# Kernel tuning notes

Measured on AMD Instinct MI355X. Metric: run time of the kernel, lower is better.

The kernel has to match this reference:

```python
import jax, jax.numpy as jnp
import numpy as np

N_NODES = 25000
N_EDGES = 400000
FEAT = 128
N_CH = 32
FEAT_OUT = 128
N_OUT = 32
P = 6
NUM_NEIGHBORS = 16.0
INV_SQRT3 = 1.0 / np.sqrt(3.0)


def _envelope_coeffs(n0, n1):
    # unique poly of degree n0+n1+1 with f(0)=1, derivs 1..n0 zero at 0,
    # f(1)=0 and derivs 1..n1 zero at 1  (== e3nn.poly_envelope(n0, n1))
    D = n0 + n1 + 1
    powers = np.arange(n0 + 1, D + 1)
    m = n1 + 1
    A = np.zeros((m, m)); b = np.zeros(m)
    for k in range(m):
        for ji, j in enumerate(powers):
            A[k, ji] = np.prod(np.arange(j, j - k, -1.0))  # falling factorial j!/(j-k)!
        b[k] = -1.0 if k == 0 else 0.0
    return powers, np.linalg.solve(A, b)

_POW, _COEF = _envelope_coeffs(P - 1, 2)


def envelope(d):
    poly = 1.0 + sum(float(c) * d ** int(j) for j, c in zip(_POW, _COEF))
    return jnp.where(d < 1.0, poly, 0.0)


def safe_norm(x, axis=None):
    x2 = jnp.sum(x ** 2, axis=axis)
    return jnp.where(x2 == 0, 1, x2) ** 0.5


def setup_inputs():
    key = jax.random.key(0)
    ks = jax.random.split(key, 10)
    x = jax.random.normal(ks[0], (N_EDGES, FEAT), jnp.float32)
    V = jax.random.normal(ks[1], (N_EDGES, N_CH, 4), jnp.float32)
    r = 0.3 * jax.random.normal(ks[2], (N_EDGES, 3), jnp.float32)  # norms mostly < cutoff 1
    Y = jax.random.normal(ks[3], (N_EDGES, 4), jnp.float32)        # irreps 0e+1o
    edge_src = jax.random.randint(ks[4], (N_EDGES,), 0, N_NODES)
    W1 = jax.random.normal(ks[5], (FEAT, N_CH), jnp.float32)
    W2a = jax.random.normal(ks[6], (FEAT + 2 * N_CH, FEAT_OUT), jnp.float32)
    W2b = jax.random.normal(ks[7], (FEAT_OUT, FEAT_OUT), jnp.float32)
    W2c = jax.random.normal(ks[8], (FEAT_OUT, FEAT_OUT), jnp.float32)
    Wlin = jax.random.normal(ks[9], (2 * N_CH, N_OUT), jnp.float32)
    return dict(x=x, V=V, r=r, Y=Y, edge_src=edge_src,
                W1=W1, W2a=W2a, W2b=W2b, W2c=W2c, Wlin=Wlin)


def reference(x, V, r, Y, edge_src, W1, W2a, W2b, W2c, Wlin):
    E, F = x.shape
    n = V.shape[1]
    d = safe_norm(r, axis=1)                               # (E,)
    # edge MLP (e3nn MLP with one layer, no activation; 1/sqrt(fan_in) weight norm)
    w = (x @ W1) / jnp.sqrt(F)                             # (E, n)
    wY = w[:, :, None] * Y[:, None, :]                     # (E, n, 4) irreps 0e+1o
    # index_add over edge_src with map_back=True
    agg = jax.ops.segment_sum(wY, edge_src, num_segments=N_NODES)
    wY = agg[edge_src] / jnp.sqrt(NUM_NEIGHBORS)           # (E, n, 4)
    # CG tensor product wY (x) V, filter_ir_out = 0e + 1o  (component normalization)
    a_s, a_v = wY[..., 0], wY[..., 1:4]
    b_s, b_v = V[..., 0], V[..., 1:4]
    s1 = a_s * b_s                                         # 0e x 0e -> 0e
    s2 = jnp.sum(a_v * b_v, axis=-1) * INV_SQRT3           # 1o x 1o -> 0e
    v1 = a_s[..., None] * b_v                              # 0e x 1o -> 1o
    v2 = a_v * b_s[..., None]                              # 1o x 0e -> 1o
    # scalars: filter(keep='0e').axis_to_mul() -> (E, 2n), concat with x
    scalars = jnp.stack([s1, s2], axis=-1).reshape(E, 2 * n)
    h = jnp.concatenate([x, scalars], axis=1)              # (E, F + 2n)
    # 3-layer silu MLP, no output activation, 1/sqrt(fan_in) weight norm
    h = jax.nn.silu((h @ W2a) / jnp.sqrt(F + 2 * n))
    h = jax.nn.silu((h @ W2b) / jnp.sqrt(FEAT_OUT))
    h = (h @ W2c) / jnp.sqrt(FEAT_OUT)
    x_out = envelope(d)[:, None] * h                       # (E, FEAT_OUT)
    # V: axis_to_mul -> (E, 2n x 1o); equivariant Linear -> n_out x 1o; mul_to_axis
    Vv = jnp.stack([v1, v2], axis=2).reshape(E, 2 * n, 3)
    V_out = jnp.einsum('eui,uv->evi', Vv, Wlin) / jnp.sqrt(2 * n)  # (E, n_out, 3)
    return x_out, V_out
```

## Files before the change

### kernel.cpp

```cpp
#include <hip/hip_runtime.h>

#define NE 400000
#define NNODES 25000

typedef __attribute__((ext_vector_type(8))) short short8;
typedef __attribute__((ext_vector_type(4))) float f32x4;

#define W2A_H 0
#define W2A_L 24576
#define W2B_H 49152
#define W2B_L 65536
#define W2C_H 81920
#define W2C_L 98304
#define WLIN_H 114688
#define WLIN_L 116736
#define W1_H   118784
#define W1_L   122880

__device__ __forceinline__ unsigned short f2bf(float f) {
  unsigned int u = __float_as_uint(f);
  unsigned int r = u + 0x7fffu + ((u >> 16) & 1u);
  return (unsigned short)(r >> 16);
}
__device__ __forceinline__ float bf2f(unsigned short h) {
  return __uint_as_float(((unsigned int)h) << 16);
}
__device__ __forceinline__ unsigned int cvtpk(float lo, float hi) {
  unsigned int r;
  asm("v_cvt_pk_bf16_f32 %0, %1, %2" : "=v"(r) : "v"(lo), "v"(hi));
  return r;
}
__device__ __forceinline__ float fsilu(float z) {
  return z * __builtin_amdgcn_rcpf(1.f + __expf(-z));
}

__global__ __launch_bounds__(256) void kscanA(const int* __restrict__ cnt,
                                              int* __restrict__ start,
                                              int* __restrict__ sums) {
  __shared__ int wtot[4];
  const int t = threadIdx.x, lane = t & 63, wid = t >> 6;
  const int idx = blockIdx.x * 256 + t;
  int v = (idx < NNODES) ? cnt[idx] : 0;
  int incl = v;
  #pragma unroll
  for (int off = 1; off < 64; off <<= 1) {
    int u = __shfl_up(incl, off, 64);
    if (lane >= off) incl += u;
  }
  if (lane == 63) wtot[wid] = incl;
  __syncthreads();
  int woff = 0;
  #pragma unroll
  for (int i = 0; i < 4; ++i)
    if (i < wid) woff += wtot[i];
  int excl = incl - v + woff;
  if (idx < NNODES) start[idx] = excl;
  if (t == 255) sums[blockIdx.x] = excl + v;
}

__global__ __launch_bounds__(64) void kscanB(int* __restrict__ sums) {
  const int lane = threadIdx.x & 63;
  int a = (lane < 98) ? sums[lane] : 0;
  int b = (64 + lane < 98) ? sums[64 + lane] : 0;
  int ia = a;
  #pragma unroll
  for (int off = 1; off < 64; off <<= 1) {
    int u = __shfl_up(ia, off, 64);
    if (lane >= off) ia += u;
  }
  int total_a = __shfl(ia, 63, 64);
  int ib = b;
  #pragma unroll
  for (int off = 1; off < 64; off <<= 1) {
    int u = __shfl_up(ib, off, 64);
    if (lane >= off) ib += u;
  }
  if (lane < 98) sums[lane] = ia - a;
  if (64 + lane < 98) sums[64 + lane] = total_a + ib - b;
}

__global__ __launch_bounds__(256) void kscanC(const int* __restrict__ sums,
                                              int* __restrict__ start,
                                              int* __restrict__ cursor) {
  const int idx = blockIdx.x * 256 + threadIdx.x;
  if (idx < NNODES) {
    int s = start[idx] + sums[blockIdx.x];
    start[idx] = s;
    cursor[idx] = s;
  }
  if (idx == 0) start[NNODES] = NE;
}

__global__ __launch_bounds__(256) void kfill(const int* __restrict__ esrc,
                                             int* __restrict__ cursor,
                                             int* __restrict__ order) {
  int e = blockIdx.x * 256 + threadIdx.x;
  if (e < NE) {
    int p = atomicAdd(&cursor[esrc[e]], 1);
    order[p] = e;
  }
}

__global__ __launch_bounds__(256) void kprep(
    const float* __restrict__ W2a, const float* __restrict__ W2b,
    const float* __restrict__ W2c, const float* __restrict__ Wlin,
    const float* __restrict__ W1, unsigned short* __restrict__ wp)
{
  int tid = blockIdx.x * 256 + threadIdx.x;
  if (tid < 7168) {
    int gi = tid;
    const float* W; float sc; unsigned short* outh; int K;
    if (gi < 3072)      { W = W2a; sc = 0.07216878364870323f; outh = wp + W2A_H; K = 192; }
    else if (gi < 5120) { W = W2b; sc = 0.08838834764831845f; outh = wp + W2B_H; K = 128; gi -= 3072; }
    else                { W = W2c; sc = 0.08838834764831845f; outh = wp + W2C_H; K = 128; gi -= 5120; }
    unsigned short* outl = outh + K * 128;
    int l15 = gi & 15, l4 = (gi >> 4) & 3, c16 = (gi >> 6) & 7, kc5 = gi >> 9;
    #pragma unroll
    for (int j = 0; j < 8; ++j) {
      int k = kc5 * 32 + l4 * 8 + j;
      int n = c16 * 16 + l15;
      float v = W[(size_t)k * 128 + n] * sc;
      unsigned short h = f2bf(v);
      outh[gi * 8 + j] = h;
      outl[gi * 8 + j] = f2bf(v - bf2f(h));
    }
  } else if (tid < 7424) {
    int gi = tid - 7168;
    int l15 = gi & 15, l4 = (gi >> 4) & 3, nt = (gi >> 6) & 1, kc2 = gi >> 7;
    #pragma unroll
    for (int j = 0; j < 8; ++j) {
      int k = kc2 * 32 + l4 * 8 + j;
      int n = nt * 16 + l15;
      float v = Wlin[(size_t)k * 32 + n] * 0.125f;
      unsigned short h = f2bf(v);
      wp[WLIN_H + gi * 8 + j] = h;
      wp[WLIN_L + gi * 8 + j] = f2bf(v - bf2f(h));
    }
  } else if (tid < 7936) {
    int gi = tid - 7424;
    int l15 = gi & 15, l4 = (gi >> 4) & 3, nf = (gi >> 6) & 1, kc5 = gi >> 7;
    #pragma unroll
    for (int j = 0; j < 8; ++j) {
      int k = kc5 * 32 + l4 * 8 + j;
      int n = nf * 16 + l15;
      float v = W1[(size_t)k * 32 + n] * 0.08838834764831845f;
      unsigned short h = f2bf(v);
      wp[W1_H + gi * 8 + j] = h;
      wp[W1_L + gi * 8 + j] = f2bf(v - bf2f(h));
    }
  }
}

__global__ __launch_bounds__(256) void k1w(
    const float* __restrict__ x, const unsigned short* __restrict__ wp,
    const int* __restrict__ esrc, int* __restrict__ cnt,
    float* __restrict__ wbuf, unsigned short* __restrict__ xh)
{
  const int t = threadIdx.x;
  const int w = t >> 6, lane = t & 63;
  const int l15 = lane & 15, l4 = lane >> 4;
  const int e0 = blockIdx.x * 128;

  if (t < 128) atomicAdd(&cnt[esrc[e0 + t]], 1);

  f32x4 acc[2][2];
  #pragma unroll
  for (int i = 0; i < 2; ++i)
    #pragma unroll
    for (int j = 0; j < 2; ++j) acc[i][j] = (f32x4)(0.f);

  #pragma unroll
  for (int kc5 = 0; kc5 < 4; ++kc5) {
    short8 bh[2], bl[2];
    #pragma unroll
    for (int nf = 0; nf < 2; ++nf) {
      int idx = (((kc5 * 2 + nf) * 4 + l4) * 16 + l15) * 8;
      bh[nf] = *(const short8*)&wp[W1_H + idx];
      bl[nf] = *(const short8*)&wp[W1_L + idx];
    }
    #pragma unroll
    for (int mf = 0; mf < 2; ++mf) {
      const int row = w * 32 + mf * 16 + l15;
      const float* xp = x + (size_t)(e0 + row) * 128 + kc5 * 32 + l4 * 8;
      float a8[8];
      *(float4*)&a8[0] = *(const float4*)xp;
      *(float4*)&a8[4] = *(const float4*)(xp + 4);
      short8 ah, al;
      #pragma unroll
      for (int j = 0; j < 8; ++j) {
        unsigned short h = f2bf(a8[j]);
        ah[j] = (short)h;
        al[j] = (short)f2bf(a8[j] - bf2f(h));
      }
      *(uint4*)&xh[(size_t)blockIdx.x * 16384 + kc5 * 4096 +
                   (w * 2 + mf) * 512 + l4 * 128 + l15 * 8] = *(uint4*)&ah;
      #pragma unroll
      for (int nf = 0; nf < 2; ++nf) {
        acc[mf][nf] = __builtin_amdgcn_mfma_f32_16x16x32_bf16(ah, bh[nf], acc[mf][nf], 0, 0, 0);
        acc[mf][nf] = __builtin_amdgcn_mfma_f32_16x16x32_bf16(ah, bl[nf], acc[mf][nf], 0, 0, 0);
        acc[mf][nf] = __builtin_amdgcn_mfma_f32_16x16x32_bf16(al, bh[nf], acc[mf][nf], 0, 0, 0);
      }
    }
  }
  #pragma unroll
  for (int mf = 0; mf < 2; ++mf)
    #pragma unroll
    for (int nf = 0; nf < 2; ++nf)
      #pragma unroll
      for (int rr = 0; rr < 4; ++rr) {
        int row = e0 + w * 32 + mf * 16 + l4 * 4 + rr;
        wbuf[(size_t)row * 32 + nf * 16 + l15] = acc[mf][nf][rr];
      }
}

__global__ __launch_bounds__(64) void k_agg(
    const float* __restrict__ wbuf, const float* __restrict__ Y,
    const int* __restrict__ start, const int* __restrict__ order,
    float* __restrict__ agg)
{
  const int n = blockIdx.x;
  const int t = threadIdx.x;
  const int c = t & 31;
  const int dh = t >> 5;
  const int s0 = start[n], s1 = start[n + 1];
  float a0 = 0.f, a1 = 0.f;
  for (int i = s0; i < s1; ++i) {
    int e = order[i];
    float wv = wbuf[(size_t)e * 32 + c];
    float y0 = Y[e * 4 + dh * 2 + 0];
    float y1 = Y[e * 4 + dh * 2 + 1];
    a0 += wv * y0;
    a1 += wv * y1;
  }
  float* ap = agg + (size_t)n * 128 + c * 4 + dh * 2;
  ap[0] = a0;
  ap[1] = a1;
}

__global__ __launch_bounds__(256, 4) void kfused(
    const unsigned short* __restrict__ xh, const float* __restrict__ V,
    const float* __restrict__ r, const int* __restrict__ esrc,
    const float* __restrict__ agg, const unsigned short* __restrict__ wp,
    float* __restrict__ xout, float* __restrict__ vout)
{
  __shared__ __align__(16) char lds[32768];

  const int t = threadIdx.x;
  const int w = t >> 6, lane = t & 63;
  const int wr = w >> 1, wc = w & 1;
  const int l15 = lane & 15, l4 = lane >> 4;
  const int e0 = blockIdx.x * 64;
  const size_t T16 = (size_t)(blockIdx.x >> 1) * 16384;
  const int xb1 = blockIdx.x & 1;

  short8 xfrag[4][2];
  #pragma unroll
  for (int kc5 = 0; kc5 < 4; ++kc5)
    #pragma unroll
    for (int mf = 0; mf < 2; ++mf)
      xfrag[kc5][mf] = *(const short8*)&xh[T16 + kc5 * 4096 + xb1 * 2048 +
                                           (wr * 2 + mf) * 512 + l4 * 128 + l15 * 8];

  {
    const int er = w * 16 + l15;
    const int e = e0 + er;
    const int src = esrc[e];
    f32x4 accv[3][2];
    #pragma unroll
    for (int i = 0; i < 3; ++i)
      #pragma unroll
      for (int nt = 0; nt < 2; ++nt) accv[i][nt] = (f32x4)(0.f);

    #pragma unroll
    for (int kc2 = 0; kc2 < 2; ++kc2) {
      short8 WhF[2], WlF[2];
      #pragma unroll
      for (int nt = 0; nt < 2; ++nt) {
        int idx = ((((kc2 * 2 + nt) * 4 + l4) * 16) + l15) * 8;
        WhF[nt] = *(const short8*)&wp[WLIN_H + idx];
        WlF[nt] = *(const short8*)&wp[WLIN_L + idx];
      }
      float4 av4[4], bv4[4];
      const float* ap = agg + (size_t)src * 128 + kc2 * 64 + l4 * 16;
      const float* bp = V + (size_t)e * 128 + kc2 * 64 + l4 * 16;
      #pragma unroll
      for (int j = 0; j < 4; ++j) {
        av4[j] = *(const float4*)(ap + j * 4);
        bv4[j] = *(const float4*)(bp + j * 4);
        av4[j].x *= 0.25f; av4[j].y *= 0.25f; av4[j].z *= 0.25f; av4[j].w *= 0.25f;
      }
      unsigned int su[4];
      #pragma unroll
      for (int ch = 0; ch < 4; ++ch) {
        float s1 = av4[ch].x * bv4[ch].x;
        float s2 = (av4[ch].y * bv4[ch].y + av4[ch].z * bv4[ch].z +
                    av4[ch].w * bv4[ch].w) * 0.5773502691896258f;
        su[ch] = cvtpk(s1, s2);
      }
      {
        int byte = er * 256 + (kc2 * 32 + l4 * 8) * 2;
        byte ^= (er & 7) << 4;
        *(uint4*)(lds + byte) = *(uint4*)su;
      }
      #pragma unroll
      for (int i = 0; i < 3; ++i) {
        union { unsigned int u[4]; short8 s; } ahu;
        #pragma unroll
        for (int ch = 0; ch < 4; ++ch) {
          float bvi = (i == 0) ? bv4[ch].y : (i == 1) ? bv4[ch].z : bv4[ch].w;
          float avi = (i == 0) ? av4[ch].y : (i == 1) ? av4[ch].z : av4[ch].w;
          ahu.u[ch] = cvtpk(av4[ch].x * bvi, avi * bv4[ch].x);
        }
        #pragma unroll
        for (int nt = 0; nt < 2; ++nt) {
          accv[i][nt] = __builtin_amdgcn_mfma_f32_16x16x32_bf16(ahu.s, WhF[nt], accv[i][nt], 0, 0, 0);
          accv[i][nt] = __builtin_amdgcn_mfma_f32_16x16x32_bf16(ahu.s, WlF[nt], accv[i][nt], 0, 0, 0);
        }
      }
    }
    const int ebase = e0 + w * 16 + l4 * 4;
    #pragma unroll
    for (int nt = 0; nt < 2; ++nt)
      #pragma unroll
      for (int rr = 0; rr < 4; ++rr) {
        float* vp = vout + (size_t)(ebase + rr) * 96 + (nt * 16 + l15) * 3;
        vp[0] = accv[0][nt][rr];
        vp[1] = accv[1][nt][rr];
        vp[2] = accv[2][nt][rr];
      }
  }

  __syncthreads();

  f32x4 acc[2][4];
  const int c16 = wc * 4;

  #pragma unroll
  for (int i = 0; i < 2; ++i)
    #pragma unroll
    for (int j = 0; j < 4; ++j) acc[i][j] = (f32x4)(0.f);

  #pragma unroll
  for (int kc5 = 0; kc5 < 6; ++kc5) {
    short8 bh[4];
    #pragma unroll
    for (int nf = 0; nf < 4; ++nf) {
      int idx = (((kc5 * 8 + c16 + nf) * 4 + l4) * 16 + l15) * 8;
      bh[nf] = *(const short8*)&wp[W2A_H + idx];
    }
    #pragma unroll
    for (int mf = 0; mf < 2; ++mf) {
      short8 ah;
      if (kc5 < 4) {
        ah = xfrag[kc5][mf];
      } else {
        int ar = wr * 32 + mf * 16 + l15;
        int byte = ar * 256 + ((kc5 - 4) * 32 + l4 * 8) * 2;
        byte ^= (ar & 7) << 4;
        ah = *(const short8*)(lds + byte);
      }
      #pragma unroll
      for (int nf = 0; nf < 4; ++nf)
        acc[mf][nf] = __builtin_amdgcn_mfma_f32_16x16x32_bf16(ah, bh[nf], acc[mf][nf], 0, 0, 0);
    }
  }

  #pragma unroll
  for (int mf = 0; mf < 2; ++mf)
    #pragma unroll
    for (int nf = 0; nf < 4; ++nf)
      #pragma unroll
      for (int rp = 0; rp < 2; ++rp) {
        unsigned int zz = cvtpk(fsilu(acc[mf][nf][2 * rp]), fsilu(acc[mf][nf][2 * rp + 1]));
        #pragma unroll
        for (int rh = 0; rh < 2; ++rh) {
          int row = wr * 32 + mf * 16 + l4 * 4 + 2 * rp + rh;
          int byte = row * 256 + (wc * 64 + nf * 16 + l15) * 2;
          byte ^= (row & 7) << 4;
          *(unsigned short*)(lds + 16384 + byte) = (unsigned short)(zz >> (16 * rh));
        }
      }

  __syncthreads();

  #pragma unroll
  for (int i = 0; i < 2; ++i)
    #pragma unroll
    for (int j = 0; j < 4; ++j) acc[i][j] = (f32x4)(0.f);

  #pragma unroll
  for (int kc5 = 0; kc5 < 4; ++kc5) {
    short8 bh[4];
    #pragma unroll
    for (int nf = 0; nf < 4; ++nf) {
      int idx = (((kc5 * 8 + c16 + nf) * 4 + l4) * 16 + l15) * 8;
      bh[nf] = *(const short8*)&wp[W2B_H + idx];
    }
    #pragma unroll
    for (int mf = 0; mf < 2; ++mf) {
      int row = wr * 32 + mf * 16 + l15;
      int byte = row * 256 + (kc5 * 32 + l4 * 8) * 2;
      byte ^= (row & 7) << 4;
      short8 ah = *(const short8*)(lds + 16384 + byte);
      #pragma unroll
      for (int nf = 0; nf < 4; ++nf)
        acc[mf][nf] = __builtin_amdgcn_mfma_f32_16x16x32_bf16(ah, bh[nf], acc[mf][nf], 0, 0, 0);
    }
  }

  #pragma unroll
  for (int mf = 0; mf < 2; ++mf)
    #pragma unroll
    for (int nf = 0; nf < 4; ++nf)
      #pragma unroll
      for (int rp = 0; rp < 2; ++rp) {
        unsigned int zz = cvtpk(fsilu(acc[mf][nf][2 * rp]), fsilu(acc[mf][nf][2 * rp + 1]));
        #pragma unroll
        for (int rh = 0; rh < 2; ++rh) {
          int row = wr * 32 + mf * 16 + l4 * 4 + 2 * rp + rh;
          int byte = row * 256 + (wc * 64 + nf * 16 + l15) * 2;
          byte ^= (row & 7) << 4;
          *(unsigned short*)(lds + byte) = (unsigned short)(zz >> (16 * rh));
        }
      }

  __syncthreads();

  #pragma unroll
  for (int i = 0; i < 2; ++i)
    #pragma unroll
    for (int j = 0; j < 4; ++j) acc[i][j] = (f32x4)(0.f);

  #pragma unroll
  for (int kc5 = 0; kc5 < 4; ++kc5) {
    short8 bh[4];
    #pragma unroll
    for (int nf = 0; nf < 4; ++nf) {
      int idx = (((kc5 * 8 + c16 + nf) * 4 + l4) * 16 + l15) * 8;
      bh[nf] = *(const short8*)&wp[W2C_H + idx];
    }
    #pragma unroll
    for (int mf = 0; mf < 2; ++mf) {
      int row = wr * 32 + mf * 16 + l15;
      int byte = row * 256 + (kc5 * 32 + l4 * 8) * 2;
      byte ^= (row & 7) << 4;
      short8 ah = *(const short8*)(lds + byte);
      #pragma unroll
      for (int nf = 0; nf < 4; ++nf)
        acc[mf][nf] = __builtin_amdgcn_mfma_f32_16x16x32_bf16(ah, bh[nf], acc[mf][nf], 0, 0, 0);
    }
  }

  #pragma unroll
  for (int mf = 0; mf < 2; ++mf) {
    float env4[4];
    #pragma unroll
    for (int rr = 0; rr < 4; ++rr) {
      int row = e0 + wr * 32 + mf * 16 + l4 * 4 + rr;
      float rx = r[row * 3 + 0];
      float ry = r[row * 3 + 1];
      float rz = r[row * 3 + 2];
      float d2 = rx * rx + ry * ry + rz * rz;
      float d = (d2 == 0.f) ? 1.f : sqrtf(d2);
      float d3 = d * d * d;
      env4[rr] = (d < 1.f) ? (1.f + d3 * d3 * (-28.f + d * (48.f - 21.f * d))) : 0.f;
    }
    #pragma unroll
    for (int nf = 0; nf < 4; ++nf)
      #pragma unroll
      for (int rr = 0; rr < 4; ++rr) {
        int row = e0 + wr * 32 + mf * 16 + l4 * 4 + rr;
        xout[(size_t)row * 128 + wc * 64 + nf * 16 + l15] = acc[mf][nf][rr] * env4[rr];
      }
  }
}

extern "C" void kernel_launch(void* const* d_in, const int* in_sizes, int n_in,
                              void* d_out, int out_size, void* d_ws, size_t ws_size,
                              hipStream_t stream)
{
  const float* x    = (const float*)d_in[0];
  const float* V    = (const float*)d_in[1];
  const float* r    = (const float*)d_in[2];
  const float* Y    = (const float*)d_in[3];
  const int*   es   = (const int*)d_in[4];
  const float* W1   = (const float*)d_in[5];
  const float* W2a  = (const float*)d_in[6];
  const float* W2b  = (const float*)d_in[7];
  const float* W2c  = (const float*)d_in[8];
  const float* Wlin = (const float*)d_in[9];

  float* ws   = (float*)d_ws;
  float* agg  = ws;
  float* wbuf = ws + 3200000;
  unsigned short* xh = (unsigned short*)(ws + 16000000);
  int*   ci   = (int*)(ws + 42000000);
  int*   cnt    = ci;
  int*   startv = ci + 25000;
  int*   cursor = ci + 50008;
  int*   order  = ci + 75008;
  int*   sums   = ci + 480000;
  unsigned short* wp = (unsigned short*)(ws + 43000000);
  float* xout = (float*)d_out;
  float* vout = (float*)d_out + 51200000;

  (void)in_sizes; (void)n_in; (void)out_size; (void)ws_size;

  hipMemsetAsync(cnt, 0, NNODES * sizeof(int), stream);
  kprep<<<dim3(31), 256, 0, stream>>>(W2a, W2b, W2c, Wlin, W1, wp);
  k1w<<<dim3(NE / 128), 256, 0, stream>>>(x, wp, es, cnt, wbuf, xh);
  kscanA<<<dim3(98), 256, 0, stream>>>(cnt, startv, sums);
  kscanB<<<dim3(1), 64, 0, stream>>>(sums);
  kscanC<<<dim3(98), 256, 0, stream>>>(sums, startv, cursor);
  kfill<<<dim3((NE + 255) / 256), 256, 0, stream>>>(es, cursor, order);
  k_agg<<<dim3(NNODES), 64, 0, stream>>>(wbuf, Y, startv, order, agg);
  kfused<<<dim3(NE / 64), 256, 0, stream>>>(xh, V, r, es, agg, wp, xout, vout);
}
```

Measured before the change: 375.1 us.

## Store edge weights as bf16, fold memset and scan pass into other kernels

Edge MLP weights w are now written as bf16 instead of fp32, halving the intermediate buffer that the gather-aggregate kernel reads. The count memset is folded into the weight-prep kernel and the single-block scan pass is merged into the final scan kernel, removing two launches. The fused kernel no longer preloads x fragments into registers and instead loads them at use, which lowers register pressure. The bf16 rounding of w adds precision loss to the aggregated values.

```diff
diff --git a/kernel.cpp b/kernel.cpp
--- a/kernel.cpp
+++ b/kernel.cpp
@@ -58,33 +58,34 @@
   if (t == 255) sums[blockIdx.x] = excl + v;
 }
 
-__global__ __launch_bounds__(64) void kscanB(int* __restrict__ sums) {
-  const int lane = threadIdx.x & 63;
-  int a = (lane < 98) ? sums[lane] : 0;
-  int b = (64 + lane < 98) ? sums[64 + lane] : 0;
-  int ia = a;
-  #pragma unroll
-  for (int off = 1; off < 64; off <<= 1) {
-    int u = __shfl_up(ia, off, 64);
-    if (lane >= off) ia += u;
-  }
-  int total_a = __shfl(ia, 63, 64);
-  int ib = b;
-  #pragma unroll
-  for (int off = 1; off < 64; off <<= 1) {
-    int u = __shfl_up(ib, off, 64);
-    if (lane >= off) ib += u;
-  }
-  if (lane < 98) sums[lane] = ia - a;
-  if (64 + lane < 98) sums[64 + lane] = total_a + ib - b;
-}
-
 __global__ __launch_bounds__(256) void kscanC(const int* __restrict__ sums,
                                               int* __restrict__ start,
                                               int* __restrict__ cursor) {
-  const int idx = blockIdx.x * 256 + threadIdx.x;
+  __shared__ int ex[128];
+  const int t = threadIdx.x, lane = t & 63;
+  if (t < 64) {
+    int a = (lane < 98) ? sums[lane] : 0;
+    int b = (64 + lane < 98) ? sums[64 + lane] : 0;
+    int ia = a;
+    #pragma unroll
+    for (int off = 1; off < 64; off <<= 1) {
+      int u = __shfl_up(ia, off, 64);
+      if (lane >= off) ia += u;
+    }
+    int total_a = __shfl(ia, 63, 64);
+    int ib = b;
+    #pragma unroll
+    for (int off = 1; off < 64; off <<= 1) {
+      int u = __shfl_up(ib, off, 64);
+      if (lane >= off) ib += u;
+    }
+    ex[lane] = ia - a;
+    ex[64 + lane] = total_a + ib - b;
+  }
+  __syncthreads();
+  const int idx = blockIdx.x * 256 + t;
   if (idx < NNODES) {
-    int s = start[idx] + sums[blockIdx.x];
+    int s = start[idx] + ex[blockIdx.x];
     start[idx] = s;
     cursor[idx] = s;
   }
@@ -104,9 +105,11 @@
 __global__ __launch_bounds__(256) void kprep(
     const float* __restrict__ W2a, const float* __restrict__ W2b,
     const float* __restrict__ W2c, const float* __restrict__ Wlin,
-    const float* __restrict__ W1, unsigned short* __restrict__ wp)
+    const float* __restrict__ W1, unsigned short* __restrict__ wp,
+    int* __restrict__ cnt)
 {
   int tid = blockIdx.x * 256 + threadIdx.x;
+  for (int i = tid; i < NNODES; i += 7936) cnt[i] = 0;
   if (tid < 7168) {
     int gi = tid;
     const float* W; float sc; unsigned short* outh; int K;
@@ -154,7 +157,7 @@
 __global__ __launch_bounds__(256) void k1w(
     const float* __restrict__ x, const unsigned short* __restrict__ wp,
     const int* __restrict__ esrc, int* __restrict__ cnt,
-    float* __restrict__ wbuf, unsigned short* __restrict__ xh)
+    unsigned short* __restrict__ wbufh, unsigned short* __restrict__ xh)
 {
   const int t = threadIdx.x;
   const int w = t >> 6, lane = t & 63;
@@ -209,12 +212,12 @@
       #pragma unroll
       for (int rr = 0; rr < 4; ++rr) {
         int row = e0 + w * 32 + mf * 16 + l4 * 4 + rr;
-        wbuf[(size_t)row * 32 + nf * 16 + l15] = acc[mf][nf][rr];
+        wbufh[(size_t)row * 32 + nf * 16 + l15] = f2bf(acc[mf][nf][rr]);
       }
 }
 
 __global__ __launch_bounds__(64) void k_agg(
-    const float* __restrict__ wbuf, const float* __restrict__ Y,
+    const unsigned short* __restrict__ wbufh, const float* __restrict__ Y,
     const int* __restrict__ start, const int* __restrict__ order,
     float* __restrict__ agg)
 {
@@ -226,7 +229,7 @@
   float a0 = 0.f, a1 = 0.f;
   for (int i = s0; i < s1; ++i) {
     int e = order[i];
-    float wv = wbuf[(size_t)e * 32 + c];
+    float wv = bf2f(wbufh[(size_t)e * 32 + c]);
     float y0 = Y[e * 4 + dh * 2 + 0];
     float y1 = Y[e * 4 + dh * 2 + 1];
     a0 += wv * y0;
@@ -252,14 +255,6 @@
   const int e0 = blockIdx.x * 64;
   const size_t T16 = (size_t)(blockIdx.x >> 1) * 16384;
   const int xb1 = blockIdx.x & 1;
-
-  short8 xfrag[4][2];
-  #pragma unroll
-  for (int kc5 = 0; kc5 < 4; ++kc5)
-    #pragma unroll
-    for (int mf = 0; mf < 2; ++mf)
-      xfrag[kc5][mf] = *(const short8*)&xh[T16 + kc5 * 4096 + xb1 * 2048 +
-                                           (wr * 2 + mf) * 512 + l4 * 128 + l15 * 8];
 
   {
     const int er = w * 16 + l15;
@@ -352,7 +347,8 @@
     for (int mf = 0; mf < 2; ++mf) {
       short8 ah;
       if (kc5 < 4) {
-        ah = xfrag[kc5][mf];
+        ah = *(const short8*)&xh[T16 + kc5 * 4096 + xb1 * 2048 +
+                                 (wr * 2 + mf) * 512 + l4 * 128 + l15 * 8];
       } else {
         int ar = wr * 32 + mf * 16 + l15;
         int byte = ar * 256 + ((kc5 - 4) * 32 + l4 * 8) * 2;
@@ -492,7 +488,7 @@
 
   float* ws   = (float*)d_ws;
   float* agg  = ws;
-  float* wbuf = ws + 3200000;
+  unsigned short* wbufh = (unsigned short*)(ws + 3200000);
   unsigned short* xh = (unsigned short*)(ws + 16000000);
   int*   ci   = (int*)(ws + 42000000);
   int*   cnt    = ci;
@@ -506,13 +502,11 @@
 
   (void)in_sizes; (void)n_in; (void)out_size; (void)ws_size;
 
-  hipMemsetAsync(cnt, 0, NNODES * sizeof(int), stream);
-  kprep<<<dim3(31), 256, 0, stream>>>(W2a, W2b, W2c, Wlin, W1, wp);
-  k1w<<<dim3(NE / 128), 256, 0, stream>>>(x, wp, es, cnt, wbuf, xh);
+  kprep<<<dim3(31), 256, 0, stream>>>(W2a, W2b, W2c, Wlin, W1, wp, cnt);
+  k1w<<<dim3(NE / 128), 256, 0, stream>>>(x, wp, es, cnt, wbufh, xh);
   kscanA<<<dim3(98), 256, 0, stream>>>(cnt, startv, sums);
-  kscanB<<<dim3(1), 64, 0, stream>>>(sums);
   kscanC<<<dim3(98), 256, 0, stream>>>(sums, startv, cursor);
   kfill<<<dim3((NE + 255) / 256), 256, 0, stream>>>(es, cursor, order);
-  k_agg<<<dim3(NNODES), 64, 0, stream>>>(wbuf, Y, startv, order, agg);
+  k_agg<<<dim3(NNODES), 64, 0, stream>>>(wbufh, Y, startv, order, agg);
   kfused<<<dim3(NE / 64), 256, 0, stream>>>(xh, V, r, es, agg, wp, xout, vout);
 }
```

New measurement: 362.0 us. -3.5%, faster.
